# Performance work log

Hardware: AMD Instinct MI355X
Metric: run time of the kernel (lower is better)

## Reference

```python
import jax, jax.numpy as jnp
import numpy as np

EMBED_DIM = 768
NUM_HEADS = 12
HEAD_DIM = EMBED_DIM // NUM_HEADS

def setup_inputs() -> dict:
    key = jax.random.key(0)
    ks = jax.random.split(key, 5)
    B, N = 16, 1024
    s_qkv = 1.0 / np.sqrt(EMBED_DIM)
    s_proj = 1.0 / np.sqrt(EMBED_DIM)
    return {
        "x": jax.random.normal(ks[0], (B, N, EMBED_DIM), dtype=jnp.float32),
        "w_qkv": jax.random.uniform(ks[1], (EMBED_DIM, 3 * EMBED_DIM), jnp.float32, -s_qkv, s_qkv),
        "b_qkv": jax.random.uniform(ks[2], (3 * EMBED_DIM,), jnp.float32, -s_qkv, s_qkv),
        "w_proj": jax.random.uniform(ks[3], (EMBED_DIM, EMBED_DIM), jnp.float32, -s_proj, s_proj),
        "b_proj": jax.random.uniform(ks[4], (EMBED_DIM,), jnp.float32, -s_proj, s_proj),
    }

def reference(x, w_qkv, b_qkv, w_proj, b_proj):
    B, N, E = x.shape
    H, D = NUM_HEADS, HEAD_DIM
    qkv = x @ w_qkv + b_qkv                       # [B, N, 3E]
    qkv = qkv.reshape(B, N, 3, H, D)
    q, k, v = jnp.moveaxis(qkv, 2, 0)             # each [B, N, H, D]
    q = jnp.swapaxes(q, 1, 2)                      # [B, H, N, D]
    k = jnp.swapaxes(k, 1, 2)
    v = jnp.swapaxes(v, 1, 2)
    attn = jnp.einsum('bhnd,bhmd->bhnm', q, k) * (D ** -0.5)
    attn = jax.nn.softmax(attn, axis=-1)
    out = jnp.einsum('bhnm,bhmd->bhnd', attn, v)   # [B, H, N, D]
    out = jnp.swapaxes(out, 1, 2).reshape(B, N, E)
    return out @ w_proj + b_proj
```

## Files before the change

kernel.cpp:

```cpp
#include <hip/hip_runtime.h>
#include <hip/hip_bf16.h>


#define EDIM 768
#define NH 12
#define HD 64
#define BB 16
#define SN 1024
#define MTOT (BB*SN)

typedef __attribute__((ext_vector_type(8))) short short8;
typedef __attribute__((ext_vector_type(4))) short short4v;
typedef __attribute__((ext_vector_type(4))) float f32x4;
typedef unsigned short bfr;

#if defined(__HIP_DEVICE_COMPILE__)
#if !__has_builtin(__builtin_amdgcn_mfma_f32_16x16x16bf16_1k)
#error "missing __builtin_amdgcn_mfma_f32_16x16x16bf16_1k on device"
#endif
#endif

#define MFMA32(A,B,C) __builtin_amdgcn_mfma_f32_16x16x32_bf16(A,B,C,0,0,0)
#define MFMA16(A,B,C) __builtin_amdgcn_mfma_f32_16x16x16bf16_1k(A,B,C,0,0,0)

__device__ __forceinline__ bfr f2bf(float f) {
    union { float f; unsigned int u; } v; v.f = f;
    unsigned int u = v.u;
    u += 0x7FFFu + ((u >> 16) & 1u);
    return (bfr)(u >> 16);
}
__device__ __forceinline__ bfr f2bf_fast(float f) {
    union { float f; unsigned int u; } v; v.f = f;
    return (bfr)((v.u + 0x8000u) >> 16);
}

__device__ __forceinline__ void gl2lds16(const bfr* g, bfr* l) {
    __builtin_amdgcn_global_load_lds(
        (__attribute__((address_space(1))) void*)(g),
        (__attribute__((address_space(3))) void*)(l), 16, 0, 0);
}

__global__ void k_convert(const float* __restrict__ in, bfr* __restrict__ out, int n4) {
    int i = blockIdx.x * blockDim.x + threadIdx.x;
    if (i >= n4) return;
    float4 v = ((const float4*)in)[i];
    ushort4 o;
    o.x = f2bf(v.x); o.y = f2bf(v.y); o.z = f2bf(v.z); o.w = f2bf(v.w);
    ((ushort4*)out)[i] = o;
}

__global__ void k_transpose_bf16(const float* __restrict__ in, bfr* __restrict__ out,
                                 int R, int C) {
    __shared__ float tile[32][33];
    int c0 = blockIdx.x * 32, r0 = blockIdx.y * 32;
    int tx = threadIdx.x & 31, ty = threadIdx.x >> 5;
    #pragma unroll
    for (int i = 0; i < 32; i += 8)
        tile[ty + i][tx] = in[(size_t)(r0 + ty + i) * C + c0 + tx];
    __syncthreads();
    #pragma unroll
    for (int i = 0; i < 32; i += 8)
        out[(size_t)(c0 + ty + i) * R + r0 + tx] = f2bf(tile[tx][ty + i]);
}

#define QSCALE 0.18033688011112042f
template <int EPI>
__launch_bounds__(256, 3)
__global__ void k_gemm_bt(const bfr* __restrict__ A, const bfr* __restrict__ BT,
                          const float* __restrict__ bias, float* __restrict__ out,
                          bfr* __restrict__ qb, bfr* __restrict__ kb, bfr* __restrict__ vT) {
    __shared__ bfr As[2][128 * 32];
    __shared__ bfr Bs[2][128 * 32];

    const int m0 = blockIdx.y * 128;
    const int n0 = blockIdx.x * 128;
    const int t = threadIdx.x;
    const int lane = t & 63;
    const int wave = t >> 6;
    const int wr = wave >> 1, wc = wave & 1;
    const int l15 = lane & 15, quad = lane >> 4;

    f32x4 acc[4][4] = {};

    const int c0 = wave * 64 + lane;
    const bfr* gA0 = A  + (size_t)(m0 + (c0 >> 2)) * 768 + (c0 & 3) * 8;
    const bfr* gA1 = A  + (size_t)(m0 + 64 + (c0 >> 2)) * 768 + (c0 & 3) * 8;
    const bfr* gB0 = BT + (size_t)(n0 + (c0 >> 2)) * 768 + (c0 & 3) * 8;
    const bfr* gB1 = BT + (size_t)(n0 + 64 + (c0 >> 2)) * 768 + (c0 & 3) * 8;
    const int w512 = wave * 512;

    for (int kt = 0; kt < 768; kt += 64) {
        __syncthreads();
        #pragma unroll
        for (int kh = 0; kh < 2; kh++) {
            const int ko = kt + kh * 32;
            gl2lds16(gA0 + ko, &As[kh][w512]);
            gl2lds16(gA1 + ko, &As[kh][2048 + w512]);
            gl2lds16(gB0 + ko, &Bs[kh][w512]);
            gl2lds16(gB1 + ko, &Bs[kh][2048 + w512]);
        }
        __syncthreads();

        #pragma unroll
        for (int kh = 0; kh < 2; kh++) {
            short8 af[4], bf[4];
            #pragma unroll
            for (int rt = 0; rt < 4; rt++)
                af[rt] = *(const short8*)(&As[kh][(wr * 64 + rt * 16 + l15) * 32 + quad * 8]);
            #pragma unroll
            for (int ct = 0; ct < 4; ct++)
                bf[ct] = *(const short8*)(&Bs[kh][(wc * 64 + ct * 16 + l15) * 32 + quad * 8]);
            #pragma unroll
            for (int rt = 0; rt < 4; rt++)
                #pragma unroll
                for (int ct = 0; ct < 4; ct++)
                    acc[rt][ct] = MFMA32(af[rt], bf[ct], acc[rt][ct]);
        }
    }

    #pragma unroll
    for (int rt = 0; rt < 4; rt++) {
        #pragma unroll
        for (int ct = 0; ct < 4; ct++) {
            const int col = n0 + wc * 64 + ct * 16 + l15;
            const float bv = bias[col];
            #pragma unroll
            for (int reg = 0; reg < 4; reg++) {
                const int m = m0 + wr * 64 + rt * 16 + quad * 4 + reg;
                float val = acc[rt][ct][reg] + bv;
                if constexpr (EPI == 0) {
                    out[(size_t)m * EDIM + col] = val;
                } else {
                    const int three = col / 768;
                    const int rem = col - three * 768;
                    const int h = rem >> 6, d = rem & 63;
                    const int b = m >> 10, n = m & 1023;
                    const size_t bh = (size_t)b * NH + h;
                    if (three == 0)      qb[(bh * SN + n) * HD + d] = f2bf(val * QSCALE);
                    else if (three == 1) kb[(bh * SN + n) * HD + d] = f2bf(val);
                    else                 vT[(bh * HD + d) * SN + n] = f2bf(val);
                }
            }
        }
    }
}

#define LDK 72

__launch_bounds__(256, 2)
__global__ void k_attn(const bfr* __restrict__ qb, const bfr* __restrict__ kb,
                       const bfr* __restrict__ vT, bfr* __restrict__ ao) {
    __shared__ bfr Ks[2][64 * LDK];
    __shared__ bfr Vs[2][64 * LDK];

    const int bh = blockIdx.x;
    const int q0 = blockIdx.y * 128;
    const int t = threadIdx.x;
    const int lane = t & 63, w = t >> 6;
    const int l15 = lane & 15, quad = lane >> 4;

    const bfr* qbase = qb + (size_t)bh * SN * HD;
    const bfr* kbase = kb + (size_t)bh * SN * HD;
    const bfr* vbase = vT + (size_t)bh * HD * SN;

    short8 qf[2][2];
    #pragma unroll
    for (int qt = 0; qt < 2; qt++)
        #pragma unroll
        for (int c = 0; c < 2; c++)
            qf[qt][c] = *(const short8*)(qbase + (size_t)(q0 + w * 32 + qt * 16 + l15) * HD + c * 32 + quad * 8);

    f32x4 o_acc[2][4] = {};
    f32x4 l_acc[2] = {};
    short4v ones4;
    #pragma unroll
    for (int i = 0; i < 4; i++) ones4[i] = (short)0x3F80;

    const int srow = t >> 2;
    const int scol = (t & 3) * 16;
    const bfr* gK = kbase + (size_t)srow * HD + scol;
    const bfr* gV = vbase + (size_t)srow * SN + scol;
    const int soff = srow * LDK + scol;

    uint4 kr0, kr1, vr0, vr1;
    kr0 = *(const uint4*)(gK);      kr1 = *(const uint4*)(gK + 8);
    vr0 = *(const uint4*)(gV);      vr1 = *(const uint4*)(gV + 8);
    *(uint4*)(&Ks[0][soff]) = kr0;  *(uint4*)(&Ks[0][soff + 8]) = kr1;
    *(uint4*)(&Vs[0][soff]) = vr0;  *(uint4*)(&Vs[0][soff + 8]) = vr1;

    for (int it = 0; it < SN / 64; it++) {
        const int cur = it & 1;
        const int kv0n = (it + 1) * 64;
        if (kv0n < SN) {
            kr0 = *(const uint4*)(gK + (size_t)kv0n * HD);
            kr1 = *(const uint4*)(gK + (size_t)kv0n * HD + 8);
            vr0 = *(const uint4*)(gV + kv0n);
            vr1 = *(const uint4*)(gV + kv0n + 8);
        }
        __syncthreads();
        if (kv0n < SN) {
            *(uint4*)(&Ks[cur ^ 1][soff]) = kr0;  *(uint4*)(&Ks[cur ^ 1][soff + 8]) = kr1;
            *(uint4*)(&Vs[cur ^ 1][soff]) = vr0;  *(uint4*)(&Vs[cur ^ 1][soff + 8]) = vr1;
        }

        const bfr* Kc = &Ks[cur][0];
        const bfr* Vc = &Vs[cur][0];

        short8 kf[4][2];
        #pragma unroll
        for (int kvt = 0; kvt < 4; kvt++)
            #pragma unroll
            for (int c = 0; c < 2; c++)
                kf[kvt][c] = *(const short8*)(Kc + (kvt * 16 + l15) * LDK + c * 32 + quad * 8);
        short4v vf[4][4];
        #pragma unroll
        for (int kvt = 0; kvt < 4; kvt++)
            #pragma unroll
            for (int ct = 0; ct < 4; ct++)
                vf[kvt][ct] = *(const short4v*)(Vc + (ct * 16 + l15) * LDK + kvt * 16 + quad * 4);

        f32x4 st[4][2] = {};
        #pragma unroll
        for (int c = 0; c < 2; c++)
            #pragma unroll
            for (int kvt = 0; kvt < 4; kvt++)
                #pragma unroll
                for (int qt = 0; qt < 2; qt++)
                    st[kvt][qt] = MFMA32(kf[kvt][c], qf[qt][c], st[kvt][qt]);

        short4v pf[4][2];
        #pragma unroll
        for (int kvt = 0; kvt < 4; kvt++)
            #pragma unroll
            for (int qt = 0; qt < 2; qt++) {
                union { unsigned u[2]; short4v s; } cv;
                cv.u[0] = (unsigned)f2bf_fast(exp2f(st[kvt][qt][0]))
                        | ((unsigned)f2bf_fast(exp2f(st[kvt][qt][1])) << 16);
                cv.u[1] = (unsigned)f2bf_fast(exp2f(st[kvt][qt][2]))
                        | ((unsigned)f2bf_fast(exp2f(st[kvt][qt][3])) << 16);
                pf[kvt][qt] = cv.s;
            }

        #pragma unroll
        for (int kvt = 0; kvt < 4; kvt++)
            #pragma unroll
            for (int qt = 0; qt < 2; qt++)
                l_acc[qt] = MFMA16(pf[kvt][qt], ones4, l_acc[qt]);
        #pragma unroll
        for (int kvt = 0; kvt < 4; kvt++)
            #pragma unroll
            for (int qt = 0; qt < 2; qt++)
                #pragma unroll
                for (int ct = 0; ct < 4; ct++)
                    o_acc[qt][ct] = MFMA16(pf[kvt][qt], vf[kvt][ct], o_acc[qt][ct]);
    }

    const int bb = bh / NH, h = bh % NH;
    #pragma unroll
    for (int qt = 0; qt < 2; qt++) {
        #pragma unroll
        for (int r = 0; r < 4; r++) {
            const float inv = 1.0f / l_acc[qt][r];
            const int n = q0 + w * 32 + qt * 16 + quad * 4 + r;
            #pragma unroll
            for (int ct = 0; ct < 4; ct++) {
                const int d = ct * 16 + l15;
                ao[((size_t)bb * SN + n) * EDIM + h * HD + d] = f2bf_fast(o_acc[qt][ct][r] * inv);
            }
        }
    }
}

extern "C" void kernel_launch(void* const* d_in, const int* in_sizes, int n_in,
                              void* d_out, int out_size, void* d_ws, size_t ws_size,
                              hipStream_t stream) {
    const float* x      = (const float*)d_in[0];
    const float* w_qkv  = (const float*)d_in[1];
    const float* b_qkv  = (const float*)d_in[2];
    const float* w_proj = (const float*)d_in[3];
    const float* b_proj = (const float*)d_in[4];

    char* ws = (char*)d_ws;
    bfr* xb     = (bfr*)(ws + 0);
    bfr* wqkvT  = (bfr*)(ws + 25165824);
    bfr* wprojT = (bfr*)(ws + 28704768);
    bfr* qb     = (bfr*)(ws + 29884416);
    bfr* kb     = (bfr*)(ws + 55050240);
    bfr* vT     = (bfr*)(ws + 80216064);
    bfr* ao     = (bfr*)(ws + 105381888);

    k_convert<<<12288, 256, 0, stream>>>(x, xb, (MTOT * EDIM) / 4);
    k_transpose_bf16<<<dim3(2304 / 32, 768 / 32), 256, 0, stream>>>(w_qkv, wqkvT, 768, 2304);
    k_transpose_bf16<<<dim3(768 / 32, 768 / 32), 256, 0, stream>>>(w_proj, wprojT, 768, 768);
    k_gemm_bt<1><<<dim3(2304 / 128, MTOT / 128), 256, 0, stream>>>(
        xb, wqkvT, b_qkv, nullptr, qb, kb, vT);
    k_attn<<<dim3(BB * NH, SN / 128), 256, 0, stream>>>(qb, kb, vT, ao);
    k_gemm_bt<0><<<dim3(768 / 128, MTOT / 128), 256, 0, stream>>>(
        ao, wprojT, b_proj, (float*)d_out, nullptr, nullptr, nullptr);
}
```

Measured before the change: 338.2 us.

## Rewrite GEMM as 256x256 tiled, swizzled-LDS, ping-pong prefetch pipeline

Replaces the 128x128, 256-thread GEMM with a 256x256 tile run by 512 threads. It double-buffers 64-wide K slices in LDS with XOR-swizzled layout and splits the loads into quarter-tile stages that overlap MFMA compute, using explicit barriers, waitcnt and setprio. It also remaps workgroup IDs in groups of 8 for cache locality. The aim is to hide global load latency and raise MFMA utilization in both the QKV and output projections. The cost is 128KB of LDS per block, fewer blocks in flight (the proj GEMM has only 192 blocks), and fragile hand-written synchronization.

```diff
diff --git a/kernel.cpp b/kernel.cpp
--- a/kernel.cpp
+++ b/kernel.cpp
@@ -39,6 +39,11 @@
         (__attribute__((address_space(1))) void*)(g),
         (__attribute__((address_space(3))) void*)(l), 16, 0, 0);
 }
+
+#define BAR()   __builtin_amdgcn_s_barrier()
+#define LGKM0() { asm volatile("s_waitcnt lgkmcnt(0)" ::: "memory"); \
+                  __builtin_amdgcn_sched_barrier(0); }
+#define VMC(n)  asm volatile("s_waitcnt vmcnt(" #n ")" ::: "memory")
 
 __global__ void k_convert(const float* __restrict__ in, bfr* __restrict__ out, int n4) {
     int i = blockIdx.x * blockDim.x + threadIdx.x;
@@ -64,70 +69,149 @@
 }
 
 #define QSCALE 0.18033688011112042f
+#define NT 12
+
 template <int EPI>
-__launch_bounds__(256, 3)
+__launch_bounds__(512, 2)
 __global__ void k_gemm_bt(const bfr* __restrict__ A, const bfr* __restrict__ BT,
                           const float* __restrict__ bias, float* __restrict__ out,
                           bfr* __restrict__ qb, bfr* __restrict__ kb, bfr* __restrict__ vT) {
-    __shared__ bfr As[2][128 * 32];
-    __shared__ bfr Bs[2][128 * 32];
-
-    const int m0 = blockIdx.y * 128;
-    const int n0 = blockIdx.x * 128;
+    __shared__ bfr As[2][256 * 64];
+    __shared__ bfr Bs[2][256 * 64];
+
+    const int gx = gridDim.x;
+    const int nwg = gx * gridDim.y;
+    int wgid = blockIdx.y * gx + blockIdx.x;
+    wgid = (wgid & 7) * (nwg >> 3) + (wgid >> 3);
+    const int n0 = (wgid % gx) * 256;
+    const int m0 = (wgid / gx) * 256;
+
     const int t = threadIdx.x;
     const int lane = t & 63;
     const int wave = t >> 6;
-    const int wr = wave >> 1, wc = wave & 1;
+    const int wr = wave >> 2;
+    const int wc = wave & 3;
     const int l15 = lane & 15, quad = lane >> 4;
 
-    f32x4 acc[4][4] = {};
-
-    const int c0 = wave * 64 + lane;
-    const bfr* gA0 = A  + (size_t)(m0 + (c0 >> 2)) * 768 + (c0 & 3) * 8;
-    const bfr* gA1 = A  + (size_t)(m0 + 64 + (c0 >> 2)) * 768 + (c0 & 3) * 8;
-    const bfr* gB0 = BT + (size_t)(n0 + (c0 >> 2)) * 768 + (c0 & 3) * 8;
-    const bfr* gB1 = BT + (size_t)(n0 + 64 + (c0 >> 2)) * 768 + (c0 & 3) * 8;
-    const int w512 = wave * 512;
-
-    for (int kt = 0; kt < 768; kt += 64) {
-        __syncthreads();
-        #pragma unroll
-        for (int kh = 0; kh < 2; kh++) {
-            const int ko = kt + kh * 32;
-            gl2lds16(gA0 + ko, &As[kh][w512]);
-            gl2lds16(gA1 + ko, &As[kh][2048 + w512]);
-            gl2lds16(gB0 + ko, &Bs[kh][w512]);
-            gl2lds16(gB1 + ko, &Bs[kh][2048 + w512]);
-        }
-        __syncthreads();
-
-        #pragma unroll
-        for (int kh = 0; kh < 2; kh++) {
-            short8 af[4], bf[4];
-            #pragma unroll
-            for (int rt = 0; rt < 4; rt++)
-                af[rt] = *(const short8*)(&As[kh][(wr * 64 + rt * 16 + l15) * 32 + quad * 8]);
-            #pragma unroll
-            for (int ct = 0; ct < 4; ct++)
-                bf[ct] = *(const short8*)(&Bs[kh][(wc * 64 + ct * 16 + l15) * 32 + quad * 8]);
-            #pragma unroll
-            for (int rt = 0; rt < 4; rt++)
-                #pragma unroll
-                for (int ct = 0; ct < 4; ct++)
-                    acc[rt][ct] = MFMA32(af[rt], bf[ct], acc[rt][ct]);
-        }
+    const int srow = t >> 3;
+    const int sg = (t & 7) ^ (srow & 7);
+    const bfr* pA = A  + (size_t)(m0 + srow) * 768 + sg * 8;
+    const bfr* pB = BT + (size_t)(n0 + srow) * 768 + sg * 8;
+    const int d0 = wave * 512;
+
+    const int pg0 = (quad ^ (l15 & 7)) * 8;
+    const int pg1 = ((4 + quad) ^ (l15 & 7)) * 8;
+    const int arow = wr * 128 + l15;
+    const int brow = wc * 64 + l15;
+
+    f32x4 acc[8][4] = {};
+    short8 a[4][2], b0[2][2], b1[2][2];
+
+#define STG_A_TOP(buf, kk) { gl2lds16(pA + (kk), &As[buf][d0]); \
+                             gl2lds16(pA + 49152 + (kk), &As[buf][4096 + d0]); }
+#define STG_A_BOT(buf, kk) { gl2lds16(pA + 98304 + (kk), &As[buf][8192 + d0]); \
+                             gl2lds16(pA + 147456 + (kk), &As[buf][12288 + d0]); }
+#define STG_B_TOP(buf, kk) { gl2lds16(pB + (kk), &Bs[buf][d0]); \
+                             gl2lds16(pB + 49152 + (kk), &Bs[buf][4096 + d0]); }
+#define STG_B_BOT(buf, kk) { gl2lds16(pB + 98304 + (kk), &Bs[buf][8192 + d0]); \
+                             gl2lds16(pB + 147456 + (kk), &Bs[buf][12288 + d0]); }
+
+    STG_A_TOP(0, 0); STG_A_BOT(0, 0); STG_B_TOP(0, 0); STG_B_BOT(0, 0);
+    STG_B_TOP(1, 64); STG_B_BOT(1, 64);
+    VMC(4);
+    BAR();
+
+    for (int c = 0; c < NT; ++c) {
+        const int cb = c & 1;
+        const bfr* Ap = &As[cb][arow * 64];
+        const bfr* Bp = &Bs[cb][brow * 64];
+        const int kn = (c + 1) * 64;
+
+        #pragma unroll
+        for (int rt = 0; rt < 4; rt++) {
+            a[rt][0] = *(const short8*)(Ap + rt * 1024 + pg0);
+            a[rt][1] = *(const short8*)(Ap + rt * 1024 + pg1);
+        }
+        #pragma unroll
+        for (int ct = 0; ct < 2; ct++) {
+            b0[ct][0] = *(const short8*)(Bp + ct * 1024 + pg0);
+            b0[ct][1] = *(const short8*)(Bp + ct * 1024 + pg1);
+        }
+        if (c + 1 < NT) STG_A_TOP(cb ^ 1, kn);
+        BAR(); LGKM0();
+        __builtin_amdgcn_s_setprio(1);
+        #pragma unroll
+        for (int rt = 0; rt < 4; rt++)
+            #pragma unroll
+            for (int ct = 0; ct < 2; ct++) {
+                acc[rt][ct] = MFMA32(a[rt][0], b0[ct][0], acc[rt][ct]);
+                acc[rt][ct] = MFMA32(a[rt][1], b0[ct][1], acc[rt][ct]);
+            }
+        __builtin_amdgcn_s_setprio(0);
+        BAR();
+
+        #pragma unroll
+        for (int ct = 0; ct < 2; ct++) {
+            b1[ct][0] = *(const short8*)(Bp + 2048 + ct * 1024 + pg0);
+            b1[ct][1] = *(const short8*)(Bp + 2048 + ct * 1024 + pg1);
+        }
+        if (c + 1 < NT) STG_A_BOT(cb ^ 1, kn);
+        BAR(); LGKM0();
+        __builtin_amdgcn_s_setprio(1);
+        #pragma unroll
+        for (int rt = 0; rt < 4; rt++)
+            #pragma unroll
+            for (int ct = 0; ct < 2; ct++) {
+                acc[rt][2 + ct] = MFMA32(a[rt][0], b1[ct][0], acc[rt][2 + ct]);
+                acc[rt][2 + ct] = MFMA32(a[rt][1], b1[ct][1], acc[rt][2 + ct]);
+            }
+        __builtin_amdgcn_s_setprio(0);
+        BAR();
+
+        #pragma unroll
+        for (int rt = 0; rt < 4; rt++) {
+            a[rt][0] = *(const short8*)(Ap + 4096 + rt * 1024 + pg0);
+            a[rt][1] = *(const short8*)(Ap + 4096 + rt * 1024 + pg1);
+        }
+        if (c + 2 < NT) STG_B_TOP(cb, kn + 64);
+        BAR(); LGKM0();
+        __builtin_amdgcn_s_setprio(1);
+        #pragma unroll
+        for (int rt = 0; rt < 4; rt++)
+            #pragma unroll
+            for (int ct = 0; ct < 2; ct++) {
+                acc[4 + rt][2 + ct] = MFMA32(a[rt][0], b1[ct][0], acc[4 + rt][2 + ct]);
+                acc[4 + rt][2 + ct] = MFMA32(a[rt][1], b1[ct][1], acc[4 + rt][2 + ct]);
+            }
+        __builtin_amdgcn_s_setprio(0);
+        BAR();
+
+        if (c + 2 < NT) STG_B_BOT(cb, kn + 64);
+        BAR();
+        __builtin_amdgcn_s_setprio(1);
+        #pragma unroll
+        for (int rt = 0; rt < 4; rt++)
+            #pragma unroll
+            for (int ct = 0; ct < 2; ct++) {
+                acc[4 + rt][ct] = MFMA32(a[rt][0], b0[ct][0], acc[4 + rt][ct]);
+                acc[4 + rt][ct] = MFMA32(a[rt][1], b0[ct][1], acc[4 + rt][ct]);
+            }
+        __builtin_amdgcn_s_setprio(0);
+        if (c < NT - 2)       { VMC(4); }
+        else if (c == NT - 2) { VMC(0); }
+        BAR();
     }
 
     #pragma unroll
-    for (int rt = 0; rt < 4; rt++) {
-        #pragma unroll
-        for (int ct = 0; ct < 4; ct++) {
-            const int col = n0 + wc * 64 + ct * 16 + l15;
+    for (int r8 = 0; r8 < 8; r8++) {
+        #pragma unroll
+        for (int c4 = 0; c4 < 4; c4++) {
+            const int col = n0 + wc * 64 + c4 * 16 + l15;
             const float bv = bias[col];
             #pragma unroll
             for (int reg = 0; reg < 4; reg++) {
-                const int m = m0 + wr * 64 + rt * 16 + quad * 4 + reg;
-                float val = acc[rt][ct][reg] + bv;
+                const int m = m0 + wr * 128 + r8 * 16 + quad * 4 + reg;
+                float val = acc[r8][c4][reg] + bv;
                 if constexpr (EPI == 0) {
                     out[(size_t)m * EDIM + col] = val;
                 } else {
@@ -292,9 +376,9 @@
     k_convert<<<12288, 256, 0, stream>>>(x, xb, (MTOT * EDIM) / 4);
     k_transpose_bf16<<<dim3(2304 / 32, 768 / 32), 256, 0, stream>>>(w_qkv, wqkvT, 768, 2304);
     k_transpose_bf16<<<dim3(768 / 32, 768 / 32), 256, 0, stream>>>(w_proj, wprojT, 768, 768);
-    k_gemm_bt<1><<<dim3(2304 / 128, MTOT / 128), 256, 0, stream>>>(
+    k_gemm_bt<1><<<dim3(2304 / 256, MTOT / 256), 512, 0, stream>>>(
         xb, wqkvT, b_qkv, nullptr, qb, kb, vT);
     k_attn<<<dim3(BB * NH, SN / 128), 256, 0, stream>>>(qb, kb, vT, ao);
-    k_gemm_bt<0><<<dim3(768 / 128, MTOT / 128), 256, 0, stream>>>(
+    k_gemm_bt<0><<<dim3(768 / 256, MTOT / 256), 512, 0, stream>>>(
         ao, wprojT, b_proj, (float*)d_out, nullptr, nullptr, nullptr);
 }
```

New measurement: 346.9 us. 2.6% more time.

## Restructure GEMM into 256x256 tiles with 4-stage LDS pipeline and swizzle

Applied to the files above, without the earlier changes.

The bf16 GEMM kernel moves from 128x128 tiles with 256 threads to 256x256 tiles with 512 threads. It adds a four-buffer LDS ring filled by global_load_lds with explicit vmcnt/lgkmcnt waits, so loads stay three k-steps ahead of compute. It also adds an XOR-like swizzle on LDS reads to avoid bank conflicts, a workgroup-ID remap across XCDs, and s_setprio around MFMA bursts. The goal is to hide global load latency and improve data reuse. In exchange, LDS use and register pressure go up and the grid has far fewer workgroups, most notably for the 768-wide projection GEMM.

```diff
diff --git a/kernel.cpp b/kernel.cpp
--- a/kernel.cpp
+++ b/kernel.cpp
@@ -39,6 +39,11 @@
         (__attribute__((address_space(1))) void*)(g),
         (__attribute__((address_space(3))) void*)(l), 16, 0, 0);
 }
+
+#define BAR()   __builtin_amdgcn_s_barrier()
+#define LGKM0() { asm volatile("s_waitcnt lgkmcnt(0)" ::: "memory"); \
+                  __builtin_amdgcn_sched_barrier(0); }
+#define VMC(n)  asm volatile("s_waitcnt vmcnt(" #n ")" ::: "memory")
 
 __global__ void k_convert(const float* __restrict__ in, bfr* __restrict__ out, int n4) {
     int i = blockIdx.x * blockDim.x + threadIdx.x;
@@ -64,70 +69,106 @@
 }
 
 #define QSCALE 0.18033688011112042f
+#define NT 24
+
 template <int EPI>
-__launch_bounds__(256, 3)
+__launch_bounds__(512, 2)
 __global__ void k_gemm_bt(const bfr* __restrict__ A, const bfr* __restrict__ BT,
                           const float* __restrict__ bias, float* __restrict__ out,
                           bfr* __restrict__ qb, bfr* __restrict__ kb, bfr* __restrict__ vT) {
-    __shared__ bfr As[2][128 * 32];
-    __shared__ bfr Bs[2][128 * 32];
-
-    const int m0 = blockIdx.y * 128;
-    const int n0 = blockIdx.x * 128;
+    __shared__ bfr As[4][256 * 32];
+    __shared__ bfr Bs[4][256 * 32];
+
+    const int gx = gridDim.x;
+    const int nwg = gx * gridDim.y;
+    int wgid = blockIdx.y * gx + blockIdx.x;
+    wgid = (wgid & 7) * (nwg >> 3) + (wgid >> 3);
+    const int n0 = (wgid % gx) * 256;
+    const int m0 = (wgid / gx) * 256;
+
     const int t = threadIdx.x;
     const int lane = t & 63;
     const int wave = t >> 6;
-    const int wr = wave >> 1, wc = wave & 1;
+    const int wr = wave >> 2;
+    const int wc = wave & 3;
     const int l15 = lane & 15, quad = lane >> 4;
 
-    f32x4 acc[4][4] = {};
-
-    const int c0 = wave * 64 + lane;
-    const bfr* gA0 = A  + (size_t)(m0 + (c0 >> 2)) * 768 + (c0 & 3) * 8;
-    const bfr* gA1 = A  + (size_t)(m0 + 64 + (c0 >> 2)) * 768 + (c0 & 3) * 8;
-    const bfr* gB0 = BT + (size_t)(n0 + (c0 >> 2)) * 768 + (c0 & 3) * 8;
-    const bfr* gB1 = BT + (size_t)(n0 + 64 + (c0 >> 2)) * 768 + (c0 & 3) * 8;
-    const int w512 = wave * 512;
-
-    for (int kt = 0; kt < 768; kt += 64) {
-        __syncthreads();
-        #pragma unroll
-        for (int kh = 0; kh < 2; kh++) {
-            const int ko = kt + kh * 32;
-            gl2lds16(gA0 + ko, &As[kh][w512]);
-            gl2lds16(gA1 + ko, &As[kh][2048 + w512]);
-            gl2lds16(gB0 + ko, &Bs[kh][w512]);
-            gl2lds16(gB1 + ko, &Bs[kh][2048 + w512]);
-        }
-        __syncthreads();
-
-        #pragma unroll
-        for (int kh = 0; kh < 2; kh++) {
-            short8 af[4], bf[4];
-            #pragma unroll
-            for (int rt = 0; rt < 4; rt++)
-                af[rt] = *(const short8*)(&As[kh][(wr * 64 + rt * 16 + l15) * 32 + quad * 8]);
+    const int srow = t >> 2;
+    const int sg = ((t & 3) - (t >> 3)) & 3;
+    const bfr* pA = A  + (size_t)(m0 + srow) * 768 + sg * 8;
+    const bfr* pB = BT + (size_t)(n0 + srow) * 768 + sg * 8;
+    const int d0 = wave * 512;
+
+    const int pg = ((quad + (l15 >> 1)) & 3) * 8;
+    const int arow = wr * 128 + l15;
+    const int brow = wc * 64 + l15;
+
+    f32x4 acc[8][4] = {};
+    short8 a[4], b[4];
+
+#define STG_A(buf, kk) { gl2lds16(pA + (kk), &As[buf][d0]); \
+                         gl2lds16(pA + 98304 + (kk), &As[buf][4096 + d0]); }
+#define STG_B(buf, kk) { gl2lds16(pB + (kk), &Bs[buf][d0]); \
+                         gl2lds16(pB + 98304 + (kk), &Bs[buf][4096 + d0]); }
+
+    STG_A(0, 0);  STG_B(0, 0);
+    STG_A(1, 32); STG_B(1, 32);
+    STG_A(2, 64); STG_B(2, 64);
+    VMC(8);
+    BAR();
+
+    for (int c = 0; c < NT; ++c) {
+        const int rb = c & 3;
+        const int sb = (c + 3) & 3;
+        const bfr* Ap = &As[rb][arow * 32];
+        const bfr* Bp = &Bs[rb][brow * 32];
+        const int kk = (c + 3) * 32;
+
+        #pragma unroll
+        for (int rf = 0; rf < 4; rf++)
+            a[rf] = *(const short8*)(Ap + rf * 512 + pg);
+        #pragma unroll
+        for (int ct = 0; ct < 4; ct++)
+            b[ct] = *(const short8*)(Bp + ct * 512 + pg);
+        if (c + 3 < NT) STG_A(sb, kk);
+        BAR(); LGKM0();
+        __builtin_amdgcn_s_setprio(1);
+        #pragma unroll
+        for (int rf = 0; rf < 4; rf++)
             #pragma unroll
             for (int ct = 0; ct < 4; ct++)
-                bf[ct] = *(const short8*)(&Bs[kh][(wc * 64 + ct * 16 + l15) * 32 + quad * 8]);
-            #pragma unroll
-            for (int rt = 0; rt < 4; rt++)
-                #pragma unroll
-                for (int ct = 0; ct < 4; ct++)
-                    acc[rt][ct] = MFMA32(af[rt], bf[ct], acc[rt][ct]);
-        }
+                acc[rf][ct] = MFMA32(a[rf], b[ct], acc[rf][ct]);
+        __builtin_amdgcn_s_setprio(0);
+        BAR();
+
+        #pragma unroll
+        for (int rf = 0; rf < 4; rf++)
+            a[rf] = *(const short8*)(Ap + 2048 + rf * 512 + pg);
+        if (c + 3 < NT) STG_B(sb, kk);
+        BAR(); LGKM0();
+        __builtin_amdgcn_s_setprio(1);
+        #pragma unroll
+        for (int rf = 0; rf < 4; rf++)
+            #pragma unroll
+            for (int ct = 0; ct < 4; ct++)
+                acc[4 + rf][ct] = MFMA32(a[rf], b[ct], acc[4 + rf][ct]);
+        __builtin_amdgcn_s_setprio(0);
+        if (c <= NT - 4)      { VMC(8); }
+        else if (c == NT - 3) { VMC(4); }
+        else if (c == NT - 2) { VMC(0); }
+        BAR();
     }
 
     #pragma unroll
-    for (int rt = 0; rt < 4; rt++) {
-        #pragma unroll
-        for (int ct = 0; ct < 4; ct++) {
-            const int col = n0 + wc * 64 + ct * 16 + l15;
+    for (int r8 = 0; r8 < 8; r8++) {
+        #pragma unroll
+        for (int c4 = 0; c4 < 4; c4++) {
+            const int col = n0 + wc * 64 + c4 * 16 + l15;
             const float bv = bias[col];
             #pragma unroll
             for (int reg = 0; reg < 4; reg++) {
-                const int m = m0 + wr * 64 + rt * 16 + quad * 4 + reg;
-                float val = acc[rt][ct][reg] + bv;
+                const int m = m0 + wr * 128 + r8 * 16 + quad * 4 + reg;
+                float val = acc[r8][c4][reg] + bv;
                 if constexpr (EPI == 0) {
                     out[(size_t)m * EDIM + col] = val;
                 } else {
@@ -292,9 +333,9 @@
     k_convert<<<12288, 256, 0, stream>>>(x, xb, (MTOT * EDIM) / 4);
     k_transpose_bf16<<<dim3(2304 / 32, 768 / 32), 256, 0, stream>>>(w_qkv, wqkvT, 768, 2304);
     k_transpose_bf16<<<dim3(768 / 32, 768 / 32), 256, 0, stream>>>(w_proj, wprojT, 768, 768);
-    k_gemm_bt<1><<<dim3(2304 / 128, MTOT / 128), 256, 0, stream>>>(
+    k_gemm_bt<1><<<dim3(2304 / 256, MTOT / 256), 512, 0, stream>>>(
         xb, wqkvT, b_qkv, nullptr, qb, kb, vT);
     k_attn<<<dim3(BB * NH, SN / 128), 256, 0, stream>>>(qb, kb, vT, ao);
-    k_gemm_bt<0><<<dim3(768 / 128, MTOT / 128), 256, 0, stream>>>(
+    k_gemm_bt<0><<<dim3(768 / 256, MTOT / 256), 512, 0, stream>>>(
         ao, wprojT, b_proj, (float*)d_out, nullptr, nullptr, nullptr);
 }
```

After: 346.5 us. 1.02x slower.
